# Kernel tuning notes

Hardware: AMD Instinct MI355X
Metric: run time of the kernel (lower is better)

Reference implementation:

```python
import jax, jax.numpy as jnp
import numpy as np

HEIGHT, WIDTH = 384, 640


def setup_inputs() -> dict:
    key = jax.random.key(0)
    ks = jax.random.split(key, 6)
    B, N, C_CLS, D = 8, 100, 92, 256
    return {
        "images": jax.random.normal(ks[0], (B, 3, HEIGHT, WIDTH), dtype=jnp.float32),
        "logits": jax.random.normal(ks[1], (B, N, C_CLS), dtype=jnp.float32),
        "pred_boxes": jax.random.uniform(ks[2], (B, N, 4), dtype=jnp.float32),
        "last_hidden_state": jax.random.normal(ks[3], (B, N, D), dtype=jnp.float32),
        "fc_w": jax.random.normal(ks[4], (256, D), dtype=jnp.float32) * 0.05,
        "fc_b": jax.random.normal(ks[5], (256,), dtype=jnp.float32) * 0.05,
    }


def reference(images, logits, pred_boxes, last_hidden_state, fc_w, fc_b):
    B = images.shape[0]
    num_objects = 2

    # probas computed in the original forward (unused in training mode -> DCE'd)
    probas = jax.nn.softmax(logits, axis=-1)[:, :, :-1]

    # cxcywh -> xyxy, scale by [W, H, W, H], truncate to int (torch .int())
    cx, cy, w, h = jnp.split(pred_boxes, 4, axis=-1)  # each [B, N, 1]
    xyxy = jnp.concatenate([cx - 0.5 * w, cy - 0.5 * h, cx + 0.5 * w, cy + 0.5 * h], axis=-1)
    img_dims = jnp.array([WIDTH, HEIGHT, WIDTH, HEIGHT], dtype=jnp.float32)
    bboxes = (xyxy * img_dims).astype(jnp.int32)  # [B, N, 4]

    # bboxes_to_mask (faithful to original, incl. its x/y axis convention):
    # x indexes rows (height), y indexes columns (width)
    x = jnp.arange(HEIGHT, dtype=jnp.float32)[:, None]   # [H, 1]
    y = jnp.arange(WIDTH, dtype=jnp.float32)[None, :]    # [1, W]
    bb = bboxes.astype(jnp.float32)[:, :, :, None, None]  # [B, N, 4, 1, 1]
    masks = (bb[:, :, 0] <= x) & (x <= bb[:, :, 2]) & (bb[:, :, 1] <= y) & (y <= bb[:, :, 3])  # [B, N, H, W]

    # diff images: sum channels, pairwise diff over (pre, post), abs, repeat x2 on batch
    summed = images.sum(axis=1).reshape(B // 2, 2, HEIGHT, WIDTH)
    diff = jnp.abs(summed[:, 1:] - summed[:, :1])          # [B/2, 1, H, W]
    diff = jnp.repeat(diff, 2, axis=0)                     # [B, 1, H, W]

    # masked mean score per box
    scores = jnp.mean(jnp.where(masks, diff, jnp.float32(0.0)), axis=(2, 3))  # [B, N]

    _, indices = jax.lax.top_k(scores, num_objects)        # [B, num_objects]
    h_i = jnp.take_along_axis(last_hidden_state, indices[:, :, None], axis=1)  # [B, O, D]
    h_i = h_i @ fc_w.T + fc_b                              # Linear: x W^T + b
    h_i = h_i.reshape(B // 2, 2, num_objects, -1)          # [b, i=2, O, hidden]
    return h_i[:, 0], h_i[:, 1]
```

## Files before the change

kernel.cpp:

```cpp
#include <hip/hip_runtime.h>

#define H_IMG 384
#define W_IMG 640
#define NPAIR 4
#define NBATCH 8
#define NBOX 100
#define DHID 256
#define ROWTILE 24
#define NTILES (H_IMG / ROWTILE)

__global__ __launch_bounds__(256) void k_sat_tile(const float* __restrict__ images,
                                                  float* __restrict__ sat,
                                                  float* __restrict__ totals_t) {
    __shared__ float buf[ROWTILE][W_IMG];

    const int p    = blockIdx.x >> 4;
    const int tile = blockIdx.x & 15;
    const int lane = threadIdx.x & 63;
    const int wv   = threadIdx.x >> 6;
    const int r_lo = tile * ROWTILE;

    const size_t chw = (size_t)H_IMG * W_IMG;

    for (int rr = wv; rr < ROWTILE; rr += 4) {
        const int h = r_lo + rr;
        const float2* i0 = (const float2*)(images + ((size_t)(2 * p)     * 3 * H_IMG + h) * W_IMG);
        const float2* i1 = (const float2*)(images + ((size_t)(2 * p + 1) * 3 * H_IMG + h) * W_IMG);
        const size_t chw2 = chw / 2;

        float carry = 0.0f;
        #pragma unroll
        for (int k = 0; k < 5; ++k) {
            const int e = k * 64 + lane;
            float2 a0 = i0[e], b0 = i0[e + chw2], c0 = i0[e + 2 * chw2];
            float2 a1 = i1[e], b1 = i1[e + chw2], c1 = i1[e + 2 * chw2];
            float dx = fabsf(((a1.x + b1.x) + c1.x) - ((a0.x + b0.x) + c0.x));
            float dy = fabsf(((a1.y + b1.y) + c1.y) - ((a0.y + b0.y) + c0.y));
            float s = dx + dy;
            #pragma unroll
            for (int off = 1; off < 64; off <<= 1) {
                float u = __shfl_up(s, off, 64);
                if (lane >= off) s += u;
            }
            const float excl = s - (dx + dy);
            buf[rr][2 * e]     = carry + excl + dx;
            buf[rr][2 * e + 1] = carry + excl + dx + dy;
            carry += __shfl(s, 63, 64);
        }
    }
    __syncthreads();

    const int t = threadIdx.x;
    #pragma unroll
    for (int sub = 0; sub < 3; ++sub) {
        const int c = sub * 256 + t;
        if (c < W_IMG) {
            float run = 0.0f;
            float* gcol = sat + ((size_t)p * H_IMG + r_lo) * W_IMG + c;
            #pragma unroll
            for (int i = 0; i < ROWTILE; ++i) {
                run += buf[i][c];
                gcol[(size_t)i * W_IMG] = run;
            }
            totals_t[((size_t)p * W_IMG + c) * NTILES + tile] = run;
        }
    }
}

__global__ __launch_bounds__(256) void k_score_topk_fc(
        const float* __restrict__ sat,
        const float* __restrict__ totals_t,
        const float* __restrict__ pred_boxes,
        const float* __restrict__ lhs,
        const float* __restrict__ fc_w,
        const float* __restrict__ fc_b,
        float* __restrict__ out) {
    const int b = blockIdx.x;
    const int t = threadIdx.x;
    const int p = b >> 1;

    __shared__ float s_off[NTILES][W_IMG];
    __shared__ float s_score[NBOX];
    __shared__ int   s_idx[2];
    __shared__ float s_h[2][DHID];

    for (int c = t; c < W_IMG; c += 256) {
        const float4* tp = (const float4*)(totals_t + ((size_t)p * W_IMG + c) * NTILES);
        float4 v0 = tp[0], v1 = tp[1], v2 = tp[2], v3 = tp[3];
        float tv[NTILES] = {v0.x, v0.y, v0.z, v0.w, v1.x, v1.y, v1.z, v1.w,
                            v2.x, v2.y, v2.z, v2.w, v3.x, v3.y, v3.z, v3.w};
        float run = 0.0f;
        #pragma unroll
        for (int tt = 0; tt < NTILES; ++tt) {
            s_off[tt][c] = run;
            run += tv[tt];
        }
    }
    __syncthreads();

    const float* S = sat + (size_t)p * H_IMG * W_IMG;

    if (t < NBOX) {
        const float* pb = pred_boxes + ((size_t)b * NBOX + t) * 4;
        const float cx = pb[0], cy = pb[1], bw = pb[2], bh = pb[3];
        const int bb0 = (int)((cx - 0.5f * bw) * 640.0f);
        const int bb1 = (int)((cy - 0.5f * bh) * 384.0f);
        const int bb2 = (int)((cx + 0.5f * bw) * 640.0f);
        const int bb3 = (int)((cy + 0.5f * bh) * 384.0f);
        const int r0 = bb0 > 0 ? bb0 : 0;
        const int r2 = bb2 < H_IMG - 1 ? bb2 : H_IMG - 1;
        const int c0 = bb1 > 0 ? bb1 : 0;
        const int c2 = bb3 < W_IMG - 1 ? bb3 : W_IMG - 1;
        float sc = 0.0f;
        if (r0 <= r2 && c0 <= c2) {
            float sum = S[(size_t)r2 * W_IMG + c2] + s_off[r2 / ROWTILE][c2];
            if (r0 > 0) sum -= S[(size_t)(r0 - 1) * W_IMG + c2] + s_off[(r0 - 1) / ROWTILE][c2];
            if (c0 > 0) sum -= S[(size_t)r2 * W_IMG + (c0 - 1)] + s_off[r2 / ROWTILE][c0 - 1];
            if (r0 > 0 && c0 > 0)
                sum += S[(size_t)(r0 - 1) * W_IMG + (c0 - 1)] + s_off[(r0 - 1) / ROWTILE][c0 - 1];
            sc = sum / (float)(H_IMG * W_IMG);
        }
        s_score[t] = sc;
    }
    __syncthreads();

    if (t == 0) {
        float b0 = -1e30f, b1 = -1e30f;
        int i0 = 0, i1 = 0;
        for (int n = 0; n < NBOX; ++n) {
            const float s = s_score[n];
            if (s > b0)      { b1 = b0; i1 = i0; b0 = s; i0 = n; }
            else if (s > b1) { b1 = s; i1 = n; }
        }
        s_idx[0] = i0;
        s_idx[1] = i1;
    }
    __syncthreads();

    s_h[0][t] = lhs[((size_t)b * NBOX + s_idx[0]) * DHID + t];
    s_h[1][t] = lhs[((size_t)b * NBOX + s_idx[1]) * DHID + t];
    __syncthreads();

    const float4* wrow4 = (const float4*)(fc_w + (size_t)t * DHID);
    float acc0 = fc_b[t];
    float acc1 = acc0;
    #pragma unroll 8
    for (int d4 = 0; d4 < DHID / 4; ++d4) {
        const float4 wv = wrow4[d4];
        const int d = d4 * 4;
        acc0 = fmaf(s_h[0][d + 0], wv.x, acc0);
        acc0 = fmaf(s_h[0][d + 1], wv.y, acc0);
        acc0 = fmaf(s_h[0][d + 2], wv.z, acc0);
        acc0 = fmaf(s_h[0][d + 3], wv.w, acc0);
        acc1 = fmaf(s_h[1][d + 0], wv.x, acc1);
        acc1 = fmaf(s_h[1][d + 1], wv.y, acc1);
        acc1 = fmaf(s_h[1][d + 2], wv.z, acc1);
        acc1 = fmaf(s_h[1][d + 3], wv.w, acc1);
    }

    const size_t base = (size_t)(b & 1) * (NPAIR * 2 * DHID) + (size_t)(b >> 1) * (2 * DHID);
    out[base + t]        = acc0;
    out[base + DHID + t] = acc1;
}

extern "C" void kernel_launch(void* const* d_in, const int* in_sizes, int n_in,
                              void* d_out, int out_size, void* d_ws, size_t ws_size,
                              hipStream_t stream) {
    const float* images     = (const float*)d_in[0];
    const float* pred_boxes = (const float*)d_in[2];
    const float* lhs        = (const float*)d_in[3];
    const float* fc_w       = (const float*)d_in[4];
    const float* fc_b       = (const float*)d_in[5];
    float* out              = (float*)d_out;

    float* sat      = (float*)d_ws;
    float* totals_t = sat + (size_t)NPAIR * H_IMG * W_IMG;

    hipLaunchKernelGGL(k_sat_tile, dim3(NPAIR * NTILES), dim3(256), 0, stream,
                       images, sat, totals_t);
    hipLaunchKernelGGL(k_score_topk_fc, dim3(NBATCH), dim3(256), 0, stream,
                       sat, totals_t, pred_boxes, lhs, fc_w, fc_b, out);
}
```

Measured before the change: 100.9 us.

## Shrink SAT row tiles, batch wave scans, and parallelize top-2 selection

Reduces the row tile from 24 to 8, so the SAT kernel launches 192 blocks instead of 64 and the score kernel builds 48 tile offsets per column. The five per-chunk wave prefix scans are interleaved to raise ILP, and results are written as float2. The serial single-thread top-2 loop becomes a wave-wide shuffle reduction with index tie-breaking. The cost is more shared offsets and more totals reads in the second kernel.

Result: faster. 92.71 us (-8.1%).

```diff
diff --git a/kernel.cpp b/kernel.cpp
--- a/kernel.cpp
+++ b/kernel.cpp
@@ -6,7 +6,7 @@
 #define NBATCH 8
 #define NBOX 100
 #define DHID 256
-#define ROWTILE 24
+#define ROWTILE 8
 #define NTILES (H_IMG / ROWTILE)
 
 __global__ __launch_bounds__(256) void k_sat_tile(const float* __restrict__ images,
@@ -14,38 +14,60 @@
                                                   float* __restrict__ totals_t) {
     __shared__ float buf[ROWTILE][W_IMG];
 
-    const int p    = blockIdx.x >> 4;
-    const int tile = blockIdx.x & 15;
+    const int p    = blockIdx.x / NTILES;
+    const int tile = blockIdx.x % NTILES;
     const int lane = threadIdx.x & 63;
     const int wv   = threadIdx.x >> 6;
     const int r_lo = tile * ROWTILE;
 
-    const size_t chw = (size_t)H_IMG * W_IMG;
+    const size_t chw  = (size_t)H_IMG * W_IMG;
+    const size_t chw2 = chw / 2;
 
     for (int rr = wv; rr < ROWTILE; rr += 4) {
         const int h = r_lo + rr;
         const float2* i0 = (const float2*)(images + ((size_t)(2 * p)     * 3 * H_IMG + h) * W_IMG);
         const float2* i1 = (const float2*)(images + ((size_t)(2 * p + 1) * 3 * H_IMG + h) * W_IMG);
-        const size_t chw2 = chw / 2;
-
-        float carry = 0.0f;
+
+        float dxv[5], dyv[5], s[5];
         #pragma unroll
         for (int k = 0; k < 5; ++k) {
             const int e = k * 64 + lane;
             float2 a0 = i0[e], b0 = i0[e + chw2], c0 = i0[e + 2 * chw2];
             float2 a1 = i1[e], b1 = i1[e + chw2], c1 = i1[e + 2 * chw2];
-            float dx = fabsf(((a1.x + b1.x) + c1.x) - ((a0.x + b0.x) + c0.x));
-            float dy = fabsf(((a1.y + b1.y) + c1.y) - ((a0.y + b0.y) + c0.y));
-            float s = dx + dy;
-            #pragma unroll
-            for (int off = 1; off < 64; off <<= 1) {
-                float u = __shfl_up(s, off, 64);
-                if (lane >= off) s += u;
+            dxv[k] = fabsf(((a1.x + b1.x) + c1.x) - ((a0.x + b0.x) + c0.x));
+            dyv[k] = fabsf(((a1.y + b1.y) + c1.y) - ((a0.y + b0.y) + c0.y));
+            s[k]   = dxv[k] + dyv[k];
+        }
+
+        #pragma unroll
+        for (int off = 1; off < 64; off <<= 1) {
+            float u0 = __shfl_up(s[0], off, 64);
+            float u1 = __shfl_up(s[1], off, 64);
+            float u2 = __shfl_up(s[2], off, 64);
+            float u3 = __shfl_up(s[3], off, 64);
+            float u4 = __shfl_up(s[4], off, 64);
+            if (lane >= off) {
+                s[0] += u0; s[1] += u1; s[2] += u2; s[3] += u3; s[4] += u4;
             }
-            const float excl = s - (dx + dy);
-            buf[rr][2 * e]     = carry + excl + dx;
-            buf[rr][2 * e + 1] = carry + excl + dx + dy;
-            carry += __shfl(s, 63, 64);
+        }
+
+        const float t0 = __shfl(s[0], 63, 64);
+        const float t1 = __shfl(s[1], 63, 64);
+        const float t2 = __shfl(s[2], 63, 64);
+        const float t3 = __shfl(s[3], 63, 64);
+        float base[5];
+        base[0] = 0.0f;
+        base[1] = t0;
+        base[2] = t0 + t1;
+        base[3] = base[2] + t2;
+        base[4] = base[3] + t3;
+
+        float2* brow = (float2*)buf[rr];
+        #pragma unroll
+        for (int k = 0; k < 5; ++k) {
+            const int e = k * 64 + lane;
+            const float excl = base[k] + s[k] - (dxv[k] + dyv[k]);
+            brow[e] = make_float2(excl + dxv[k], excl + dxv[k] + dyv[k]);
         }
     }
     __syncthreads();
@@ -86,14 +108,14 @@
 
     for (int c = t; c < W_IMG; c += 256) {
         const float4* tp = (const float4*)(totals_t + ((size_t)p * W_IMG + c) * NTILES);
-        float4 v0 = tp[0], v1 = tp[1], v2 = tp[2], v3 = tp[3];
-        float tv[NTILES] = {v0.x, v0.y, v0.z, v0.w, v1.x, v1.y, v1.z, v1.w,
-                            v2.x, v2.y, v2.z, v2.w, v3.x, v3.y, v3.z, v3.w};
         float run = 0.0f;
         #pragma unroll
-        for (int tt = 0; tt < NTILES; ++tt) {
-            s_off[tt][c] = run;
-            run += tv[tt];
+        for (int q = 0; q < NTILES / 4; ++q) {
+            const float4 v = tp[q];
+            s_off[q * 4 + 0][c] = run; run += v.x;
+            s_off[q * 4 + 1][c] = run; run += v.y;
+            s_off[q * 4 + 2][c] = run; run += v.z;
+            s_off[q * 4 + 3][c] = run; run += v.w;
         }
     }
     __syncthreads();
@@ -113,27 +135,45 @@
         const int c2 = bb3 < W_IMG - 1 ? bb3 : W_IMG - 1;
         float sc = 0.0f;
         if (r0 <= r2 && c0 <= c2) {
-            float sum = S[(size_t)r2 * W_IMG + c2] + s_off[r2 / ROWTILE][c2];
-            if (r0 > 0) sum -= S[(size_t)(r0 - 1) * W_IMG + c2] + s_off[(r0 - 1) / ROWTILE][c2];
-            if (c0 > 0) sum -= S[(size_t)r2 * W_IMG + (c0 - 1)] + s_off[r2 / ROWTILE][c0 - 1];
+            float sum = S[(size_t)r2 * W_IMG + c2] + s_off[r2 >> 3][c2];
+            if (r0 > 0) sum -= S[(size_t)(r0 - 1) * W_IMG + c2] + s_off[(r0 - 1) >> 3][c2];
+            if (c0 > 0) sum -= S[(size_t)r2 * W_IMG + (c0 - 1)] + s_off[r2 >> 3][c0 - 1];
             if (r0 > 0 && c0 > 0)
-                sum += S[(size_t)(r0 - 1) * W_IMG + (c0 - 1)] + s_off[(r0 - 1) / ROWTILE][c0 - 1];
+                sum += S[(size_t)(r0 - 1) * W_IMG + (c0 - 1)] + s_off[(r0 - 1) >> 3][c0 - 1];
             sc = sum / (float)(H_IMG * W_IMG);
         }
         s_score[t] = sc;
     }
     __syncthreads();
 
-    if (t == 0) {
-        float b0 = -1e30f, b1 = -1e30f;
-        int i0 = 0, i1 = 0;
-        for (int n = 0; n < NBOX; ++n) {
-            const float s = s_score[n];
-            if (s > b0)      { b1 = b0; i1 = i0; b0 = s; i0 = n; }
-            else if (s > b1) { b1 = s; i1 = n; }
-        }
-        s_idx[0] = i0;
-        s_idx[1] = i1;
+    if (t < 64) {
+        float b0 = s_score[t];
+        int   i0 = t;
+        float b1 = -1e30f;
+        int   i1 = 0x7fffffff;
+        if (t + 64 < NBOX) {
+            const float s1 = s_score[t + 64];
+            if (s1 > b0) { b1 = b0; i1 = i0; b0 = s1; i0 = t + 64; }
+            else         { b1 = s1; i1 = t + 64; }
+        }
+        #pragma unroll
+        for (int off = 32; off > 0; off >>= 1) {
+            const float o0 = __shfl_xor(b0, off, 64);
+            const float o1 = __shfl_xor(b1, off, 64);
+            const int   j0 = __shfl_xor(i0, off, 64);
+            const int   j1 = __shfl_xor(i1, off, 64);
+            const bool other_first = (o0 > b0) || (o0 == b0 && j0 < i0);
+            if (other_first) {
+                const bool mine2 = (b0 > o1) || (b0 == o1 && i0 < j1);
+                const float n1 = mine2 ? b0 : o1;
+                const int  nj1 = mine2 ? i0 : j1;
+                b0 = o0; i0 = j0; b1 = n1; i1 = nj1;
+            } else {
+                const bool oth2 = (o0 > b1) || (o0 == b1 && j0 < i1);
+                if (oth2) { b1 = o0; i1 = j0; }
+            }
+        }
+        if (t == 0) { s_idx[0] = i0; s_idx[1] = i1; }
     }
     __syncthreads();
 
```
